# Performance work log

Measured on AMD Instinct MI355X. Metric: run time of the kernel, lower is better.

The kernel has to match this reference:

```python
import jax, jax.numpy as jnp
import numpy as np

N = 2048      # layer_size
R = 4         # displacement rank
B = 4096      # batch
STD = 0.01    # init_stddev


def toeplitz_mult(G, H, x):
    """out[b] = sum_i Krylov(Z_1, g_i) @ Krylov(Z_{-1}, h_i)^T @ x[b]   (cycle=True, f=(1,-1)).

    Krylov(Z_1, g) is the circulant matrix C(g) with first column g:
        C(g)[i, j] = g[(i-j) mod n]
    Krylov(Z_{-1}, h) is the skew-circulant S(h):
        S(h)[i, j] = h[(i-j) mod n] * (-1 if i < j else 1)
    Using the factorization S(h) = D^{-1} C(D h) D with D = diag(eta^k), eta = exp(i*pi/n):
        S(h)^T x = D C((D h)') D^{-1} x,   where c'[k] = c[(-k) mod n]
    and circulant products are done via FFT: C(c) u = ifft(fft(c) * fft(u)).
    """
    r, n = G.shape
    eta = jnp.exp(1j * jnp.pi * jnp.arange(n) / n).astype(jnp.complex64)  # (n,)
    # ---- transpose Krylov multiply with f = -1:  U_i = S(h_i)^T x,  shape (r, b, n) ----
    Hm = H.astype(jnp.complex64) * eta                      # D h_i, (r, n)
    Hm_rev = jnp.roll(Hm[:, ::-1], 1, axis=-1)              # c'[k] = c[(-k) mod n]
    xm = x.astype(jnp.complex64) / eta                      # D^{-1} x, (b, n)
    U = jnp.fft.ifft(jnp.fft.fft(Hm_rev)[:, None, :] * jnp.fft.fft(xm)[None, :, :], axis=-1)
    U = (U * eta).real                                      # S(h_i)^T x is real, (r, b, n)
    # ---- Krylov multiply with f = 1:  Y_i = C(g_i) U_i ----
    Gf = jnp.fft.fft(G.astype(jnp.complex64))[:, None, :]   # (r, 1, n)
    Y = jnp.fft.ifft(Gf * jnp.fft.fft(U.astype(jnp.complex64), axis=-1), axis=-1).real
    return Y.sum(0)                                         # (b, n)


def setup_inputs() -> dict:
    key = jax.random.key(0)
    k1, k2, k3 = jax.random.split(key, 3)
    x = jax.random.normal(k1, (B, N), jnp.float32)
    G = jax.random.normal(k2, (R, N), jnp.float32) * STD
    H = jax.random.normal(k3, (R, N), jnp.float32) * STD
    return {"x": x, "G": G, "H": H}


def reference(x, G, H):
    return toeplitz_mult(G, H, x)
```

## Files before the change

### kernel.cpp

```cpp
#include <hip/hip_runtime.h>
#include <cstdint>
#include <cstddef>

constexpr int kN = 2048;
constexpr int kB = 4096;
constexpr int kR = 4;

typedef __attribute__((ext_vector_type(4))) float f32x4;
typedef __attribute__((ext_vector_type(8))) short short8;
typedef __attribute__((ext_vector_type(8))) unsigned short ushort8;

__device__ __forceinline__ unsigned short f2bf(float f) {
  unsigned u = __float_as_uint(f);
  u += 0x7FFFu + ((u >> 16) & 1u);
  return (unsigned short)(u >> 16);
}

__device__ __forceinline__ void gload_lds16(const void* g, void* l) {
  __builtin_amdgcn_global_load_lds(
      (const __attribute__((address_space(1))) void*)g,
      (__attribute__((address_space(3))) void*)l, 16, 0, 0);
}

__global__ void prep_kernel(const float* __restrict__ x,
                            const float* __restrict__ G,
                            const float* __restrict__ H,
                            unsigned short* __restrict__ xb,
                            unsigned short* __restrict__ Dp) {
  __shared__ float wsum[4];
  const int tid = threadIdx.x;

  if (blockIdx.x < (kB * kN) / (256 * 8)) {
    const int t = blockIdx.x * 256 + tid;
    const float4* xv = (const float4*)x;
    float4 a = xv[t * 2];
    float4 b = xv[t * 2 + 1];
    ushort8 o;
    o[0] = f2bf(a.x); o[1] = f2bf(a.y); o[2] = f2bf(a.z); o[3] = f2bf(a.w);
    o[4] = f2bf(b.x); o[5] = f2bf(b.y); o[6] = f2bf(b.z); o[7] = f2bf(b.w);
    *(ushort8*)(xb + (size_t)t * 8) = o;
    return;
  }

  const int d = blockIdx.x - (kB * kN) / (256 * 8);
  const int lane = tid & 63, wave = tid >> 6;
  const int v0 = tid * 8;

  float loc[8];
  float run = 0.f;
#pragma unroll
  for (int jj = 0; jj < 8; ++jj) {
    const int v = v0 + jj;
    float q = 0.f;
#pragma unroll
    for (int t = 0; t < kR; ++t)
      q += G[t * kN + ((v + d) & (kN - 1))] * H[t * kN + v];
    run += q;
    loc[jj] = run;
  }

  float incl = run;
#pragma unroll
  for (int off = 1; off < 64; off <<= 1) {
    float tv = __shfl_up(incl, off, 64);
    if (lane >= off) incl += tv;
  }
  if (lane == 63) wsum[wave] = incl;
  __syncthreads();
  float woff = 0.f, total = 0.f;
#pragma unroll
  for (int w = 0; w < 4; ++w) {
    const float s = wsum[w];
    total += s;
    if (w < wave) woff += s;
  }
  const float exc = woff + incl - run;

  ushort8 o;
#pragma unroll
  for (int jj = 0; jj < 8; ++jj)
    o[jj] = f2bf(2.f * (exc + loc[jj]) - total);
  *(ushort8*)(Dp + (size_t)d * kN + v0) = o;
}

__global__ void build_M_kernel(const unsigned short* __restrict__ Dp,
                               unsigned short* __restrict__ Mb) {
  __shared__ unsigned short lds[128][64];
  const int tid = threadIdx.x;
  const int i0 = blockIdx.y * 64, j0 = blockIdx.x * 64;
  const int delta0 = (i0 - j0 - 63) & (kN - 1);
#pragma unroll
  for (int it = 0; it < 32; ++it) {
    const int lin = it * 256 + tid;
    const int dd = lin >> 6, jj = lin & 63;
    lds[dd][jj] = Dp[(size_t)((delta0 + dd) & (kN - 1)) * kN + j0 + jj];
  }
  __syncthreads();
#pragma unroll
  for (int it = 0; it < 16; ++it) {
    const int lin = it * 256 + tid;
    const int ii = lin >> 6, jj = lin & 63;
    Mb[(size_t)(i0 + ii) * kN + j0 + jj] = lds[ii - jj + 63][jj];
  }
}

__global__ __launch_bounds__(256) void gemm_kernel(
    const unsigned short* __restrict__ A,
    const unsigned short* __restrict__ Bt,
    float* __restrict__ C) {
  __shared__ unsigned short As[128][32];
  __shared__ unsigned short Bs[64][32];

  const int tid = threadIdx.x;
  const int lane = tid & 63, wave = tid >> 6;
  const int wr = wave >> 1, wc = wave & 1;
  const int r16 = lane & 15, kg = lane >> 4;

  const int flat = blockIdx.y * gridDim.x + blockIdx.x;
  const int swz = (flat & 7) * 128 + (flat >> 3);
  const int by = swz >> 5, bx = swz & 31;
  const int row0 = by * 128;
  const int col0 = bx * 64;

  f32x4 acc[4][2] = {};

  const int srow = tid >> 2;
  const int scol = (tid & 3) * 8;

  for (int k0 = 0; k0 < kN; k0 += 32) {
    __syncthreads();
#pragma unroll
    for (int s = 0; s < 2; ++s)
      gload_lds16(A + (size_t)(row0 + s * 64 + srow) * kN + k0 + scol,
                  (char*)As + s * 4096 + wave * 1024);
    gload_lds16(Bt + (size_t)(col0 + srow) * kN + k0 + scol,
                (char*)Bs + wave * 1024);
    __syncthreads();

    short8 af[4], bf[2];
#pragma unroll
    for (int mt = 0; mt < 4; ++mt)
      af[mt] = *(const short8*)&As[wr * 64 + mt * 16 + r16][kg * 8];
#pragma unroll
    for (int nt = 0; nt < 2; ++nt)
      bf[nt] = *(const short8*)&Bs[wc * 32 + nt * 16 + r16][kg * 8];
#pragma unroll
    for (int mt = 0; mt < 4; ++mt)
#pragma unroll
      for (int nt = 0; nt < 2; ++nt)
        acc[mt][nt] = __builtin_amdgcn_mfma_f32_16x16x32_bf16(
            af[mt], bf[nt], acc[mt][nt], 0, 0, 0);
  }

#pragma unroll
  for (int mt = 0; mt < 4; ++mt)
#pragma unroll
    for (int nt = 0; nt < 2; ++nt) {
      const int r = row0 + wr * 64 + mt * 16 + kg * 4;
      const int c = col0 + wc * 32 + nt * 16 + r16;
#pragma unroll
      for (int j = 0; j < 4; ++j)
        C[(size_t)(r + j) * kN + c] = acc[mt][nt][j];
    }
}

extern "C" void kernel_launch(void* const* d_in, const int* in_sizes, int n_in,
                              void* d_out, int out_size, void* d_ws, size_t ws_size,
                              hipStream_t stream) {
  const float* x = (const float*)d_in[0];
  const float* G = (const float*)d_in[1];
  const float* H = (const float*)d_in[2];
  float* out = (float*)d_out;

  char* ws = (char*)d_ws;
  unsigned short* Mb = (unsigned short*)ws;
  unsigned short* xb = (unsigned short*)(ws + (8u << 20));
  unsigned short* Dp = (unsigned short*)(ws + (24u << 20));

  const int cast_blocks = (kB * kN) / (256 * 8);
  prep_kernel<<<dim3(cast_blocks + kN), dim3(256), 0, stream>>>(x, G, H, xb, Dp);
  build_M_kernel<<<dim3(kN / 64, kN / 64), dim3(256), 0, stream>>>(Dp, Mb);
  gemm_kernel<<<dim3(kN / 64, kB / 128), dim3(256), 0, stream>>>(xb, Mb, out);
}
```

Measured before the change: 175.5 us.

## Enlarge GEMM tile to 128x128 with double-buffered LDS and swizzled layout

```diff
diff --git a/kernel.cpp b/kernel.cpp
--- a/kernel.cpp
+++ b/kernel.cpp
@@ -108,8 +108,8 @@
     const unsigned short* __restrict__ A,
     const unsigned short* __restrict__ Bt,
     float* __restrict__ C) {
-  __shared__ unsigned short As[128][32];
-  __shared__ unsigned short Bs[64][32];
+  __shared__ unsigned short As[2][8192];
+  __shared__ unsigned short Bs[2][8192];
 
   const int tid = threadIdx.x;
   const int lane = tid & 63, wave = tid >> 6;
@@ -117,47 +117,71 @@
   const int r16 = lane & 15, kg = lane >> 4;
 
   const int flat = blockIdx.y * gridDim.x + blockIdx.x;
-  const int swz = (flat & 7) * 128 + (flat >> 3);
-  const int by = swz >> 5, bx = swz & 31;
-  const int row0 = by * 128;
-  const int col0 = bx * 64;
-
-  f32x4 acc[4][2] = {};
-
-  const int srow = tid >> 2;
-  const int scol = (tid & 3) * 8;
-
-  for (int k0 = 0; k0 < kN; k0 += 32) {
+  const int swz = (flat & 7) * 64 + (flat >> 3);
+  const int by = swz >> 4, bx = swz & 15;
+  const int row0 = by * 128, col0 = bx * 128;
+
+  const unsigned short* Abase = A + (size_t)row0 * kN;
+  const unsigned short* Bbase = Bt + (size_t)col0 * kN;
+  const int ldsw = wave * 1024;
+
+  f32x4 acc[4][4] = {};
+
+  auto stage = [&](const unsigned short* src, unsigned short* dstbase) {
+#pragma unroll
+    for (int i = 0; i < 4; ++i) {
+      const int r = (i & 1) * 64 + (tid >> 2);
+      const int gbyte = r * (kN * 2) + (i >> 1) * 64
+                        + (((tid & 3) ^ (r & 3)) * 16);
+      gload_lds16((const char*)src + gbyte, (char*)dstbase + i * 4096 + ldsw);
+    }
+  };
+
+  stage(Abase, As[0]);
+  stage(Bbase, Bs[0]);
+  __syncthreads();
+
+  for (int t = 0; t < kN / 64; ++t) {
+    const int cur = t & 1;
+    if (t < kN / 64 - 1) {
+      stage(Abase + (t + 1) * 64, As[cur ^ 1]);
+      stage(Bbase + (t + 1) * 64, Bs[cur ^ 1]);
+    }
+    __builtin_amdgcn_sched_barrier(0);
+
+    short8 af[2][4], bf[2][4];
+#pragma unroll
+    for (int s = 0; s < 2; ++s)
+#pragma unroll
+      for (int mt = 0; mt < 4; ++mt) {
+        const int row = wr * 64 + mt * 16 + r16;
+        af[s][mt] = *(const short8*)&As[cur][s * 4096 + row * 32 + ((kg ^ (row & 3)) << 3)];
+      }
+#pragma unroll
+    for (int s = 0; s < 2; ++s)
+#pragma unroll
+      for (int nt = 0; nt < 4; ++nt) {
+        const int row = wc * 64 + nt * 16 + r16;
+        bf[s][nt] = *(const short8*)&Bs[cur][s * 4096 + row * 32 + ((kg ^ (row & 3)) << 3)];
+      }
+#pragma unroll
+    for (int mt = 0; mt < 4; ++mt)
+#pragma unroll
+      for (int nt = 0; nt < 4; ++nt)
+#pragma unroll
+        for (int s = 0; s < 2; ++s)
+          acc[mt][nt] = __builtin_amdgcn_mfma_f32_16x16x32_bf16(
+              af[s][mt], bf[s][nt], acc[mt][nt], 0, 0, 0);
+
     __syncthreads();
-#pragma unroll
-    for (int s = 0; s < 2; ++s)
-      gload_lds16(A + (size_t)(row0 + s * 64 + srow) * kN + k0 + scol,
-                  (char*)As + s * 4096 + wave * 1024);
-    gload_lds16(Bt + (size_t)(col0 + srow) * kN + k0 + scol,
-                (char*)Bs + wave * 1024);
-    __syncthreads();
-
-    short8 af[4], bf[2];
-#pragma unroll
-    for (int mt = 0; mt < 4; ++mt)
-      af[mt] = *(const short8*)&As[wr * 64 + mt * 16 + r16][kg * 8];
-#pragma unroll
-    for (int nt = 0; nt < 2; ++nt)
-      bf[nt] = *(const short8*)&Bs[wc * 32 + nt * 16 + r16][kg * 8];
-#pragma unroll
-    for (int mt = 0; mt < 4; ++mt)
-#pragma unroll
-      for (int nt = 0; nt < 2; ++nt)
-        acc[mt][nt] = __builtin_amdgcn_mfma_f32_16x16x32_bf16(
-            af[mt], bf[nt], acc[mt][nt], 0, 0, 0);
   }
 
 #pragma unroll
   for (int mt = 0; mt < 4; ++mt)
 #pragma unroll
-    for (int nt = 0; nt < 2; ++nt) {
+    for (int nt = 0; nt < 4; ++nt) {
       const int r = row0 + wr * 64 + mt * 16 + kg * 4;
-      const int c = col0 + wc * 32 + nt * 16 + r16;
+      const int c = col0 + wc * 64 + nt * 16 + r16;
 #pragma unroll
       for (int j = 0; j < 4; ++j)
         C[(size_t)(r + j) * kN + c] = acc[mt][nt][j];
@@ -180,5 +204,5 @@
   const int cast_blocks = (kB * kN) / (256 * 8);
   prep_kernel<<<dim3(cast_blocks + kN), dim3(256), 0, stream>>>(x, G, H, xb, Dp);
   build_M_kernel<<<dim3(kN / 64, kN / 64), dim3(256), 0, stream>>>(Dp, Mb);
-  gemm_kernel<<<dim3(kN / 64, kB / 128), dim3(256), 0, stream>>>(xb, Mb, out);
-}
+  gemm_kernel<<<dim3(kN / 128, kB / 128), dim3(256), 0, stream>>>(xb, Mb, out);
+}
```

After: 165.9 us. -5.5%, faster.

## Double-buffer GEMM LDS tiles with K=64 steps and XOR-swizzled layout

Applied to the files above, without the earlier changes.

```diff
diff --git a/kernel.cpp b/kernel.cpp
--- a/kernel.cpp
+++ b/kernel.cpp
@@ -104,12 +104,12 @@
   }
 }
 
-__global__ __launch_bounds__(256) void gemm_kernel(
+__global__ __launch_bounds__(256, 3) void gemm_kernel(
     const unsigned short* __restrict__ A,
     const unsigned short* __restrict__ Bt,
     float* __restrict__ C) {
-  __shared__ unsigned short As[128][32];
-  __shared__ unsigned short Bs[64][32];
+  __shared__ unsigned short As[2][8192];
+  __shared__ unsigned short Bs[2][4096];
 
   const int tid = threadIdx.x;
   const int lane = tid & 63, wave = tid >> 6;
@@ -119,37 +119,68 @@
   const int flat = blockIdx.y * gridDim.x + blockIdx.x;
   const int swz = (flat & 7) * 128 + (flat >> 3);
   const int by = swz >> 5, bx = swz & 31;
-  const int row0 = by * 128;
-  const int col0 = bx * 64;
+  const int row0 = by * 128, col0 = bx * 64;
+
+  const unsigned short* Abase = A + (size_t)row0 * kN;
+  const unsigned short* Bbase = Bt + (size_t)col0 * kN;
 
   f32x4 acc[4][2] = {};
 
-  const int srow = tid >> 2;
-  const int scol = (tid & 3) * 8;
-
-  for (int k0 = 0; k0 < kN; k0 += 32) {
+  auto stageA = [&](const unsigned short* src, unsigned short* dst) {
+#pragma unroll
+    for (int i = 0; i < 4; ++i) {
+      const int slot = i * 256 + tid;
+      const int r = slot >> 3, cl = slot & 7;
+      gload_lds16((const char*)src + r * (kN * 2) + ((cl ^ (r & 7)) << 4),
+                  (char*)dst + slot * 16);
+    }
+  };
+  auto stageB = [&](const unsigned short* src, unsigned short* dst) {
+#pragma unroll
+    for (int i = 0; i < 2; ++i) {
+      const int slot = i * 256 + tid;
+      const int r = slot >> 3, cl = slot & 7;
+      gload_lds16((const char*)src + r * (kN * 2) + ((cl ^ (r & 7)) << 4),
+                  (char*)dst + slot * 16);
+    }
+  };
+
+  stageA(Abase, As[0]);
+  stageB(Bbase, Bs[0]);
+  __syncthreads();
+
+  for (int t = 0; t < kN / 64; ++t) {
+    const int cur = t & 1;
+    if (t < kN / 64 - 1) {
+      stageA(Abase + (t + 1) * 64, As[cur ^ 1]);
+      stageB(Bbase + (t + 1) * 64, Bs[cur ^ 1]);
+    }
+    __builtin_amdgcn_sched_barrier(0);
+
+    const char* abuf = (const char*)As[cur];
+    const char* bbuf = (const char*)Bs[cur];
+#pragma unroll
+    for (int s = 0; s < 2; ++s) {
+      short8 af[4], bf[2];
+#pragma unroll
+      for (int mt = 0; mt < 4; ++mt) {
+        const int row = wr * 64 + mt * 16 + r16;
+        af[mt] = *(const short8*)(abuf + row * 128 + (((s * 4 + kg) ^ (row & 7)) << 4));
+      }
+#pragma unroll
+      for (int nt = 0; nt < 2; ++nt) {
+        const int row = wc * 32 + nt * 16 + r16;
+        bf[nt] = *(const short8*)(bbuf + row * 128 + (((s * 4 + kg) ^ (row & 7)) << 4));
+      }
+#pragma unroll
+      for (int mt = 0; mt < 4; ++mt)
+#pragma unroll
+        for (int nt = 0; nt < 2; ++nt)
+          acc[mt][nt] = __builtin_amdgcn_mfma_f32_16x16x32_bf16(
+              af[mt], bf[nt], acc[mt][nt], 0, 0, 0);
+    }
+
     __syncthreads();
-#pragma unroll
-    for (int s = 0; s < 2; ++s)
-      gload_lds16(A + (size_t)(row0 + s * 64 + srow) * kN + k0 + scol,
-                  (char*)As + s * 4096 + wave * 1024);
-    gload_lds16(Bt + (size_t)(col0 + srow) * kN + k0 + scol,
-                (char*)Bs + wave * 1024);
-    __syncthreads();
-
-    short8 af[4], bf[2];
-#pragma unroll
-    for (int mt = 0; mt < 4; ++mt)
-      af[mt] = *(const short8*)&As[wr * 64 + mt * 16 + r16][kg * 8];
-#pragma unroll
-    for (int nt = 0; nt < 2; ++nt)
-      bf[nt] = *(const short8*)&Bs[wc * 32 + nt * 16 + r16][kg * 8];
-#pragma unroll
-    for (int mt = 0; mt < 4; ++mt)
-#pragma unroll
-      for (int nt = 0; nt < 2; ++nt)
-        acc[mt][nt] = __builtin_amdgcn_mfma_f32_16x16x32_bf16(
-            af[mt], bf[nt], acc[mt][nt], 0, 0, 0);
   }
 
 #pragma unroll
```

After: 178.2 us. No clear change (+1.6%).

## Rewrite GEMM with 256x256 tiles, double-buffered swizzled LDS and split-K atomics

Applied to the files above, without the earlier changes.

```diff
diff --git a/kernel.cpp b/kernel.cpp
--- a/kernel.cpp
+++ b/kernel.cpp
@@ -104,64 +104,125 @@
   }
 }
 
-__global__ __launch_bounds__(256) void gemm_kernel(
+__global__ void zero_out_kernel(float4* __restrict__ out4) {
+  const int i = blockIdx.x * blockDim.x + threadIdx.x;
+  out4[i * 2]     = float4{0.f, 0.f, 0.f, 0.f};
+  out4[i * 2 + 1] = float4{0.f, 0.f, 0.f, 0.f};
+}
+
+__global__ __launch_bounds__(512, 2) void gemm_kernel(
     const unsigned short* __restrict__ A,
     const unsigned short* __restrict__ Bt,
     float* __restrict__ C) {
-  __shared__ unsigned short As[128][32];
-  __shared__ unsigned short Bs[64][32];
+  __shared__ unsigned short As[2][2][128 * 64];
+  __shared__ unsigned short Bs[2][2][128 * 64];
 
   const int tid = threadIdx.x;
   const int lane = tid & 63, wave = tid >> 6;
-  const int wr = wave >> 1, wc = wave & 1;
   const int r16 = lane & 15, kg = lane >> 4;
-
-  const int flat = blockIdx.y * gridDim.x + blockIdx.x;
-  const int swz = (flat & 7) * 128 + (flat >> 3);
-  const int by = swz >> 5, bx = swz & 31;
-  const int row0 = by * 128;
-  const int col0 = bx * 64;
-
-  f32x4 acc[4][2] = {};
-
-  const int srow = tid >> 2;
-  const int scol = (tid & 3) * 8;
-
-  for (int k0 = 0; k0 < kN; k0 += 32) {
-    __syncthreads();
-#pragma unroll
-    for (int s = 0; s < 2; ++s)
-      gload_lds16(A + (size_t)(row0 + s * 64 + srow) * kN + k0 + scol,
-                  (char*)As + s * 4096 + wave * 1024);
-    gload_lds16(Bt + (size_t)(col0 + srow) * kN + k0 + scol,
-                (char*)Bs + wave * 1024);
-    __syncthreads();
-
-    short8 af[4], bf[2];
-#pragma unroll
-    for (int mt = 0; mt < 4; ++mt)
-      af[mt] = *(const short8*)&As[wr * 64 + mt * 16 + r16][kg * 8];
-#pragma unroll
-    for (int nt = 0; nt < 2; ++nt)
-      bf[nt] = *(const short8*)&Bs[wc * 32 + nt * 16 + r16][kg * 8];
-#pragma unroll
-    for (int mt = 0; mt < 4; ++mt)
-#pragma unroll
-      for (int nt = 0; nt < 2; ++nt)
-        acc[mt][nt] = __builtin_amdgcn_mfma_f32_16x16x32_bf16(
-            af[mt], bf[nt], acc[mt][nt], 0, 0, 0);
-  }
-
-#pragma unroll
-  for (int mt = 0; mt < 4; ++mt)
-#pragma unroll
-    for (int nt = 0; nt < 2; ++nt) {
-      const int r = row0 + wr * 64 + mt * 16 + kg * 4;
-      const int c = col0 + wc * 32 + nt * 16 + r16;
-#pragma unroll
-      for (int j = 0; j < 4; ++j)
-        C[(size_t)(r + j) * kN + c] = acc[mt][nt][j];
-    }
+  const int mrow0 = (wave >> 2) * 64;
+  const int ncol0 = (wave & 3) * 32;
+
+  const int row0 = blockIdx.y * 256;
+  const int col0 = blockIdx.x * 256;
+  const int kz = blockIdx.z;
+
+  const char* Abase = (const char*)(A + (size_t)row0 * kN + kz * 1024);
+  const char* Bbase = (const char*)(Bt + (size_t)col0 * kN + kz * 1024);
+
+  int goff[2];
+#pragma unroll
+  for (int i = 0; i < 2; ++i) {
+    const int r = i * 64 + (tid >> 3), c = tid & 7;
+    goff[i] = r * (kN * 2) + ((c ^ (r & 7)) << 4);
+  }
+
+  f32x4 acc[4][4][2] = {};
+
+#define STG(MAT, BUF, H, KT)                                                   \
+  { _Pragma("unroll")                                                          \
+    for (int i = 0; i < 2; ++i)                                                \
+      gload_lds16(MAT##base + (H) * 128 * (kN * 2) + (KT) * 128 + goff[i],     \
+                  (char*)&MAT##s[BUF][H][0] + (i * 512 + tid) * 16); }
+
+#define PH(BUF, QM, QN, Q, STGCODE, WTCODE)                                    \
+  {                                                                            \
+    WTCODE;                                   \
+    __builtin_amdgcn_s_barrier();              \
+    const char* ab = (const char*)&As[BUF][QM][0];                             \
+    const char* bb = (const char*)&Bs[BUF][QN][0];                             \
+    short8 a_[2][4], b_[2][2];                                                 \
+    _Pragma("unroll")                                                          \
+    for (int ks = 0; ks < 2; ++ks) {                                           \
+      _Pragma("unroll")                                                        \
+      for (int mf = 0; mf < 4; ++mf) {                                         \
+        const int row = mrow0 + mf * 16 + r16;                                 \
+        a_[ks][mf] = *(const short8*)(ab + row * 128 +                         \
+                                      (((ks * 4 + kg) ^ (row & 7)) << 4));     \
+      }                                                                        \
+      _Pragma("unroll")                                                        \
+      for (int nf = 0; nf < 2; ++nf) {                                         \
+        const int row = ncol0 + nf * 16 + r16;                                 \
+        b_[ks][nf] = *(const short8*)(bb + row * 128 +                         \
+                                      (((ks * 4 + kg) ^ (row & 7)) << 4));     \
+      }                                                                        \
+    }                                                                          \
+    STGCODE;                                         \
+    asm volatile("s_waitcnt lgkmcnt(0)" ::: "memory");                         \
+    __builtin_amdgcn_sched_barrier(0);                                         \
+    __builtin_amdgcn_s_setprio(1);                                             \
+    _Pragma("unroll")                                                          \
+    for (int ks = 0; ks < 2; ++ks)                                             \
+      _Pragma("unroll")                                                        \
+      for (int mf = 0; mf < 4; ++mf)                                           \
+        _Pragma("unroll")                                                      \
+        for (int nf = 0; nf < 2; ++nf)                                         \
+          acc[Q][mf][nf] = __builtin_amdgcn_mfma_f32_16x16x32_bf16(            \
+              a_[ks][mf], b_[ks][nf], acc[Q][mf][nf], 0, 0, 0);                \
+    __builtin_amdgcn_s_setprio(0);                                             \
+  }
+
+#define VM(N) asm volatile("s_waitcnt vmcnt(" #N ")" ::: "memory")
+
+  STG(A, 0, 0, 0);
+  STG(B, 0, 0, 0);
+  STG(A, 0, 1, 0);
+  STG(B, 0, 1, 0);
+  STG(A, 1, 0, 1);
+  STG(B, 1, 0, 1);
+
+  const int NIT = 1024 / 128;
+  for (int it = 0; it < NIT; ++it) {
+    const int t1 = 2 * it + 1, t2 = 2 * it + 2, t3 = 2 * it + 3;
+    const bool more = (it + 1) < NIT;
+
+    PH(0, 0, 0, 0, STG(A, 1, 1, t1), VM(8));
+    PH(0, 0, 1, 1, STG(B, 1, 1, t1), VM(6));
+    PH(0, 1, 0, 2, if (more) STG(A, 0, 0, t2), );
+    PH(0, 1, 1, 3, if (more) STG(B, 0, 0, t2), );
+    PH(1, 0, 0, 0, if (more) STG(A, 0, 1, t2), if (more) VM(8); else VM(4));
+    PH(1, 0, 1, 1, if (more) STG(B, 0, 1, t2), if (more) VM(6); else VM(0));
+    PH(1, 1, 0, 2, if (more) STG(A, 1, 0, t3), );
+    PH(1, 1, 1, 3, if (more) STG(B, 1, 0, t3), );
+  }
+#undef PH
+#undef STG
+#undef VM
+
+#pragma unroll
+  for (int q = 0; q < 4; ++q) {
+    const int qm = q >> 1, qn = q & 1;
+#pragma unroll
+    for (int mf = 0; mf < 4; ++mf)
+#pragma unroll
+      for (int nf = 0; nf < 2; ++nf) {
+        const int r = row0 + qm * 128 + mrow0 + mf * 16 + kg * 4;
+        const int c = col0 + qn * 128 + ncol0 + nf * 16 + r16;
+#pragma unroll
+        for (int j = 0; j < 4; ++j)
+          atomicAdd(&C[(size_t)(r + j) * kN + c], acc[q][mf][nf][j]);
+      }
+  }
 }
 
 extern "C" void kernel_launch(void* const* d_in, const int* in_sizes, int n_in,
@@ -180,5 +241,6 @@
   const int cast_blocks = (kB * kN) / (256 * 8);
   prep_kernel<<<dim3(cast_blocks + kN), dim3(256), 0, stream>>>(x, G, H, xb, Dp);
   build_M_kernel<<<dim3(kN / 64, kN / 64), dim3(256), 0, stream>>>(Dp, Mb);
-  gemm_kernel<<<dim3(kN / 64, kB / 128), dim3(256), 0, stream>>>(xb, Mb, out);
-}
+  zero_out_kernel<<<dim3((kB * kN) / (256 * 8)), dim3(256), 0, stream>>>((float4*)out);
+  gemm_kernel<<<dim3(kN / 256, kB / 256, 2), dim3(512), 0, stream>>>(xb, Mb, out);
+}
```

Result: slower. 214.5 us (+22.2%).
